# Performance work log

Measured on AMD Instinct MI355X. Metric: run time of the kernel, lower is better.

The kernel has to match this reference:

```python
import jax, jax.numpy as jnp
import numpy as np

B, S, D, H = 4, 2048, 1024, 16
HD = D // H  # 64


def setup_inputs() -> dict:
    key = jax.random.key(0)
    ks = jax.random.split(key, 8)
    s = 0.02
    return {
        "inp_values": jax.random.normal(ks[0], (B, S, D), jnp.float32),
        "inp_keys": jax.random.normal(ks[1], (B, S, D), jnp.float32),
        "inp_queries": jax.random.normal(ks[2], (B, S, D), jnp.float32),
        # per-head projection weights, torch nn.Linear(head_dims, head_dims, bias=False): y = x @ W.T
        "Wv": jax.random.normal(ks[3], (HD, HD), jnp.float32) * s,
        "Wk": jax.random.normal(ks[4], (HD, HD), jnp.float32) * s,
        "Wq": jax.random.normal(ks[5], (HD, HD), jnp.float32) * s,
        # output projection nn.Linear(D, D) with bias
        "Wo": jax.random.normal(ks[6], (D, D), jnp.float32) * s,
        "bo": jax.random.normal(ks[7], (D,), jnp.float32) * s,
    }


def reference(inp_values, inp_keys, inp_queries, Wv, Wk, Wq, Wo, bo):
    b, sq, _ = inp_queries.shape
    sk = inp_values.shape[1]
    v = inp_values.reshape(b, sk, H, HD)
    k = inp_keys.reshape(b, sk, H, HD)
    q = inp_queries.reshape(b, sq, H, HD)
    # per-head linear: x @ W.T
    v = jnp.einsum('bshd,ed->bshe', v, Wv)
    k = jnp.einsum('bshd,ed->bshe', k, Wk)
    q = jnp.einsum('bshd,ed->bshe', q, Wq)
    # scores scaled by 1/sqrt(input_dims) as in the original (not head_dims)
    scores = jnp.einsum('bqhd,bkhd->bhqk', q, k) / jnp.sqrt(jnp.float32(D))
    attn = jax.nn.softmax(scores, axis=-1)  # [B,H,Q,K]
    out = jnp.einsum('bhqk,bkhd->bqhd', attn, v).reshape(b, sq, D)
    return out @ Wo.T + bo
```

## Files before the change

### kernel.cpp

```cpp
#include <hip/hip_runtime.h>
#include <hip/hip_bf16.h>

#define B_ 4
#define S_ 2048
#define D_ 1024
#define H_ 16
#define HD_ 64

typedef __attribute__((ext_vector_type(8))) short bf16x8;
typedef __attribute__((ext_vector_type(4))) float f32x4;

#define MFMA32(a, b, c) __builtin_amdgcn_mfma_f32_16x16x32_bf16(a, b, c, 0, 0, 0)

#define KSWZ(r) ((((r) & 3)) ^ ((((r) >> 3) & 1) << 2))

__device__ __forceinline__ float fast_exp2(float x) {
#if __has_builtin(__builtin_amdgcn_exp2f)
  return __builtin_amdgcn_exp2f(x);
#else
  return exp2f(x);
#endif
}

__device__ __forceinline__ float fast_rcp(float x) {
#if __has_builtin(__builtin_amdgcn_rcpf)
  return __builtin_amdgcn_rcpf(x);
#else
  return 1.0f / x;
#endif
}

__device__ __forceinline__ short f2bf(float x) {
  union { float f; unsigned u; } v; v.f = x;
  unsigned r = (v.u + 0x7fffu + ((v.u >> 16) & 1u)) >> 16;
  return (short)(r & 0xffffu);
}

__device__ __forceinline__ unsigned pack_hi16(float a, float b) {
  union { float f; unsigned u; } ua, ub; ua.f = a; ub.f = b;
  return __builtin_amdgcn_perm(ub.u, ua.u, 0x07060302u);
}

__device__ __forceinline__ void gl_lds16(const short* g, void* l) {
  __builtin_amdgcn_global_load_lds(
      (const __attribute__((address_space(1))) unsigned*)(const void*)g,
      (__attribute__((address_space(3))) unsigned*)l, 16, 0, 0);
}

__global__ __launch_bounds__(256) void qkv_proj2(
    const float* __restrict__ inpV, const float* __restrict__ inpK,
    const float* __restrict__ inpQ, const float* __restrict__ Wv,
    const float* __restrict__ Wk, const float* __restrict__ Wq,
    const float* __restrict__ Wo, short* __restrict__ wob,
    short* __restrict__ vt, short* __restrict__ kp, short* __restrict__ qp) {
  __shared__ bf16x8 xbuf[1024];
  __shared__ bf16x8 wbuf[512];
  int bid = blockIdx.x;
  int t = bid >> 10;
  int tid = threadIdx.x, wave = tid >> 6, lane = tid & 63;
  int quad = lane >> 4, l15 = lane & 15;

  if (t == 3) {
    int i = (bid & 511) * 256 + tid;
    const float4* src = (const float4*)Wo + i * 2;
    float4 a = src[0], b = src[1];
    bf16x8 o;
    o[0] = f2bf(a.x); o[1] = f2bf(a.y); o[2] = f2bf(a.z); o[3] = f2bf(a.w);
    o[4] = f2bf(b.x); o[5] = f2bf(b.y); o[6] = f2bf(b.z); o[7] = f2bf(b.w);
    ((bf16x8*)wob)[i] = o;
    return;
  }

  int bh = (bid >> 4) & 63;
  int st = bid & 15;
  int b = bh >> 4, h = bh & 15;
  int s0 = st * 128;
  const float* inp = (t == 0) ? inpV : (t == 1) ? inpK : inpQ;
  const float* W = (t == 0) ? Wv : (t == 1) ? Wk : Wq;
  float wscale = (t == 2) ? (0.03125f * 1.4426950408889634f) : 1.0f;

#pragma unroll
  for (int u = 0; u < 2; ++u) {
    int slot = tid + u * 256;
    int row = slot >> 3, g = slot & 7;
    const float4* wp = (const float4*)(W + row * 64 + g * 8);
    float4 w0 = wp[0], w1 = wp[1];
    bf16x8 o;
    o[0] = f2bf(w0.x * wscale); o[1] = f2bf(w0.y * wscale);
    o[2] = f2bf(w0.z * wscale); o[3] = f2bf(w0.w * wscale);
    o[4] = f2bf(w1.x * wscale); o[5] = f2bf(w1.y * wscale);
    o[6] = f2bf(w1.z * wscale); o[7] = f2bf(w1.w * wscale);
    wbuf[row * 8 + (g ^ (row & 7))] = o;
  }
  const float* xg = inp + (b * S_ + s0) * D_ + h * HD_;
#pragma unroll
  for (int u = 0; u < 4; ++u) {
    int slot = tid + u * 256;
    int row = slot >> 3, g = slot & 7;
    const float4* xp = (const float4*)(xg + row * D_ + g * 8);
    float4 x0 = xp[0], x1 = xp[1];
    bf16x8 o;
    o[0] = f2bf(x0.x); o[1] = f2bf(x0.y); o[2] = f2bf(x0.z); o[3] = f2bf(x0.w);
    o[4] = f2bf(x1.x); o[5] = f2bf(x1.y); o[6] = f2bf(x1.z); o[7] = f2bf(x1.w);
    xbuf[row * 8 + (g ^ (row & 7))] = o;
  }
  __syncthreads();

  if (t == 0) {
    f32x4 acc[4][2];
#pragma unroll
    for (int mt = 0; mt < 4; mt++)
#pragma unroll
      for (int nt = 0; nt < 2; nt++) { acc[mt][nt][0]=0.f; acc[mt][nt][1]=0.f; acc[mt][nt][2]=0.f; acc[mt][nt][3]=0.f; }
#pragma unroll
    for (int ks = 0; ks < 2; ++ks) {
      bf16x8 af[4], bfr[2];
#pragma unroll
      for (int mt = 0; mt < 4; ++mt) {
        int row = mt * 16 + l15;
        af[mt] = wbuf[row * 8 + ((ks * 4 + quad) ^ (row & 7))];
      }
#pragma unroll
      for (int nt = 0; nt < 2; ++nt) {
        int row = wave * 32 + nt * 16 + l15;
        bfr[nt] = xbuf[row * 8 + ((ks * 4 + quad) ^ (row & 7))];
      }
#pragma unroll
      for (int mt = 0; mt < 4; ++mt)
#pragma unroll
        for (int nt = 0; nt < 2; ++nt)
          acc[mt][nt] = MFMA32(af[mt], bfr[nt], acc[mt][nt]);
    }
    short* vb = vt + (bh * 64) * S_ + s0 + wave * 32;
#pragma unroll
    for (int mt = 0; mt < 4; ++mt)
#pragma unroll
      for (int nt = 0; nt < 2; ++nt)
#pragma unroll
        for (int r = 0; r < 4; ++r) {
          int e = mt * 16 + quad * 4 + r;
          int s = nt * 16 + l15;
          vb[e * S_ + s] = f2bf(acc[mt][nt][r]);
        }
  } else {
    f32x4 acc[2][4];
#pragma unroll
    for (int mt = 0; mt < 2; mt++)
#pragma unroll
      for (int nt = 0; nt < 4; nt++) { acc[mt][nt][0]=0.f; acc[mt][nt][1]=0.f; acc[mt][nt][2]=0.f; acc[mt][nt][3]=0.f; }
#pragma unroll
    for (int ks = 0; ks < 2; ++ks) {
      bf16x8 af[2], bfr[4];
#pragma unroll
      for (int mt = 0; mt < 2; ++mt) {
        int row = wave * 32 + mt * 16 + l15;
        af[mt] = xbuf[row * 8 + ((ks * 4 + quad) ^ (row & 7))];
      }
#pragma unroll
      for (int nt = 0; nt < 4; ++nt) {
        int row = nt * 16 + l15;
        bfr[nt] = wbuf[row * 8 + ((ks * 4 + quad) ^ (row & 7))];
      }
#pragma unroll
      for (int mt = 0; mt < 2; ++mt)
#pragma unroll
        for (int nt = 0; nt < 4; ++nt)
          acc[mt][nt] = MFMA32(af[mt], bfr[nt], acc[mt][nt]);
    }
    short* ob = ((t == 1) ? kp : qp) + (bh * S_ + s0 + wave * 32) * 64;
#pragma unroll
    for (int mt = 0; mt < 2; ++mt)
#pragma unroll
      for (int nt = 0; nt < 4; ++nt)
#pragma unroll
        for (int r = 0; r < 4; ++r) {
          int s = mt * 16 + quad * 4 + r;
          int e = nt * 16 + l15;
          ob[s * 64 + e] = f2bf(acc[mt][nt][r]);
        }
  }
}

__global__ __launch_bounds__(128, 4) void attention(
    const short* __restrict__ qp, const short* __restrict__ kp,
    const short* __restrict__ vt, short* __restrict__ ao) {
  __shared__ bf16x8 kbuf[2][256];
  __shared__ bf16x8 vbuf[2][256];
  int bid = blockIdx.x;
  int qt = bid >> 6;
  int bh = bid & 63;
  int tid = threadIdx.x, wave = tid >> 6, lane = tid & 63;
  int quad = lane >> 4, l15 = lane & 15;

  const short* qb = qp + (bh * S_ + qt * 64 + wave * 32 + l15) * 64;
  bf16x8 bq[2][2];
  bq[0][0] = *(const bf16x8*)(qb + quad * 8);
  bq[0][1] = *(const bf16x8*)(qb + 32 + quad * 8);
  bq[1][0] = *(const bf16x8*)(qb + 1024 + quad * 8);
  bq[1][1] = *(const bf16x8*)(qb + 1024 + 32 + quad * 8);

  const f32x4 fzero = {0.f, 0.f, 0.f, 0.f};
  f32x4 o[2][4];
#pragma unroll
  for (int g = 0; g < 2; g++)
#pragma unroll
    for (int dt = 0; dt < 4; dt++) o[g][dt] = fzero;
  f32x4 lacc[2];
  lacc[0] = fzero; lacc[1] = fzero;

  short one_bf = (short)0x3F80;
  bf16x8 ones8;
#pragma unroll
  for (int j = 0; j < 8; ++j) ones8[j] = (l15 == 0) ? one_bf : (short)0;

  const short* kg = kp + bh * S_ * 64;
  const short* vg = vt + bh * 64 * S_;

  int krow0 = tid >> 3, kg0 = (tid & 7) ^ KSWZ(krow0);
  int krow1 = (tid + 128) >> 3, kg1 = (tid & 7) ^ KSWZ(krow1);
  const short* kA = kg + krow0 * 64 + kg0 * 8;
  const short* kB = kg + krow1 * 64 + kg1 * 8;
  int vrow0 = tid >> 2, vg0 = (tid & 3) ^ (vrow0 & 3);
  int vrow1 = (tid + 128) >> 2, vg1 = (tid & 3) ^ (vrow1 & 3);
  const short* vA = vg + vrow0 * S_ + vg0 * 8;
  const short* vB = vg + vrow1 * S_ + vg1 * 8;

  gl_lds16(kA, &kbuf[0][tid]);
  gl_lds16(kB, &kbuf[0][tid + 128]);
  gl_lds16(vA, &vbuf[0][tid]);
  gl_lds16(vB, &vbuf[0][tid + 128]);

  int krp0 = ((l15 >> 2) << 3) + (l15 & 3);

  int aslot0[2], aslot1[2], vslot[4];
#pragma unroll
  for (int nt = 0; nt < 2; ++nt) {
    int krow = krp0 + nt * 4;
    aslot0[nt] = krow * 8 + ((0 + quad) ^ KSWZ(krow));
    aslot1[nt] = krow * 8 + ((4 + quad) ^ KSWZ(krow));
  }
#pragma unroll
  for (int dt = 0; dt < 4; ++dt) {
    int d = dt * 16 + l15;
    vslot[dt] = d * 4 + (quad ^ (d & 3));
  }

#define ATTN_BODY(P, T)                                                     \
  do {                                                                      \
    __syncthreads();                                                        \
    int ktn = ((T) + 1) & 63;                                               \
    gl_lds16(kA + ktn * 2048, &kbuf[(P) ^ 1][tid]);                         \
    gl_lds16(kB + ktn * 2048, &kbuf[(P) ^ 1][tid + 128]);                   \
    gl_lds16(vA + ktn * 32, &vbuf[(P) ^ 1][tid]);                           \
    gl_lds16(vB + ktn * 32, &vbuf[(P) ^ 1][tid + 128]);                     \
    union Frag { unsigned u[4]; bf16x8 v; } pa0, pa1;                       \
    _Pragma("unroll")                                                       \
    for (int nt = 0; nt < 2; ++nt) {                                        \
      bf16x8 ak0 = kbuf[(P)][aslot0[nt]];                                   \
      bf16x8 ak1 = kbuf[(P)][aslot1[nt]];                                   \
      f32x4 c0 = MFMA32(ak0, bq[0][0], fzero);                              \
      f32x4 c1 = MFMA32(ak0, bq[1][0], fzero);                              \
      c0 = MFMA32(ak1, bq[0][1], c0);                                       \
      c1 = MFMA32(ak1, bq[1][1], c1);                                       \
      float e00 = fast_exp2(c0[0]), e01 = fast_exp2(c0[1]);                 \
      float e02 = fast_exp2(c0[2]), e03 = fast_exp2(c0[3]);                 \
      float e10 = fast_exp2(c1[0]), e11 = fast_exp2(c1[1]);                 \
      float e12 = fast_exp2(c1[2]), e13 = fast_exp2(c1[3]);                 \
      pa0.u[nt * 2 + 0] = pack_hi16(e00, e01);                              \
      pa0.u[nt * 2 + 1] = pack_hi16(e02, e03);                              \
      pa1.u[nt * 2 + 0] = pack_hi16(e10, e11);                              \
      pa1.u[nt * 2 + 1] = pack_hi16(e12, e13);                              \
    }                                                                       \
    __builtin_amdgcn_s_setprio(1);                                          \
    lacc[0] = MFMA32(pa0.v, ones8, lacc[0]);                                \
    lacc[1] = MFMA32(pa1.v, ones8, lacc[1]);                                \
    _Pragma("unroll")                                                       \
    for (int dt = 0; dt < 4; ++dt) {                                        \
      bf16x8 bv = vbuf[(P)][vslot[dt]];                                     \
      o[0][dt] = MFMA32(pa0.v, bv, o[0][dt]);                               \
      o[1][dt] = MFMA32(pa1.v, bv, o[1][dt]);                               \
    }                                                                       \
    __builtin_amdgcn_s_setprio(0);                                          \
  } while (0)

  for (int kt = 0; kt < 64; kt += 2) {
    ATTN_BODY(0, kt);
    ATTN_BODY(1, kt + 1);
  }
#undef ATTN_BODY

  int b = bh >> 4, h = bh & 15;
#pragma unroll
  for (int g = 0; g < 2; ++g) {
    float inv[4];
#pragma unroll
    for (int r = 0; r < 4; ++r) {
      float ls = __shfl(lacc[g][r], lane & 48, 64);
      inv[r] = fast_rcp(ls);
    }
#pragma unroll
    for (int dt = 0; dt < 4; ++dt)
#pragma unroll
      for (int r = 0; r < 4; ++r) {
        int srow = qt * 64 + wave * 32 + g * 16 + quad * 4 + r;
        ao[(b * S_ + srow) * D_ + h * 64 + dt * 16 + l15] =
            f2bf(o[g][dt][r] * inv[r]);
      }
  }
}

__global__ __launch_bounds__(256) void outproj(const short* __restrict__ A,
                                               const short* __restrict__ Bw,
                                               const float* __restrict__ bo,
                                               float* __restrict__ out) {
  __shared__ bf16x8 sa[2][1024];
  __shared__ bf16x8 sb[2][1024];
  int bid = blockIdx.x;
  int m0 = (bid >> 3) * 128, n0 = (bid & 7) * 128;
  int tid = threadIdx.x, wave = tid >> 6, lane = tid & 63;
  int quad = lane >> 4, l15 = lane & 15;
  int wm = (wave >> 1) * 64, wn = (wave & 1) * 64;
  f32x4 acc[4][4];
#pragma unroll
  for (int mt = 0; mt < 4; mt++)
#pragma unroll
    for (int nt = 0; nt < 4; nt++) { acc[mt][nt][0]=0.f; acc[mt][nt][1]=0.f; acc[mt][nt][2]=0.f; acc[mt][nt][3]=0.f; }

  const short* asrc[4];
  const short* bsrc[4];
#pragma unroll
  for (int u = 0; u < 4; ++u) {
    int slot = tid + u * 256;
    int row = slot >> 3, g = (slot & 7) ^ (row & 7);
    asrc[u] = A + (m0 + row) * 1024 + g * 8;
    bsrc[u] = Bw + (n0 + row) * 1024 + g * 8;
  }
#pragma unroll
  for (int u = 0; u < 4; ++u) {
    gl_lds16(asrc[u], &sa[0][tid + u * 256]);
    gl_lds16(bsrc[u], &sb[0][tid + u * 256]);
  }

  int p = 0;
  for (int k0 = 0; k0 < 1024; k0 += 64) {
    __syncthreads();
    int kn = (k0 + 64) & 1023;
#pragma unroll
    for (int u = 0; u < 4; ++u) {
      gl_lds16(asrc[u] + kn, &sa[p ^ 1][tid + u * 256]);
      gl_lds16(bsrc[u] + kn, &sb[p ^ 1][tid + u * 256]);
    }
#pragma unroll
    for (int ks = 0; ks < 2; ++ks) {
      bf16x8 af[4], bf[4];
#pragma unroll
      for (int mt = 0; mt < 4; ++mt) {
        int row = wm + mt * 16 + l15;
        af[mt] = sa[p][row * 8 + ((ks * 4 + quad) ^ (row & 7))];
      }
#pragma unroll
      for (int nt = 0; nt < 4; ++nt) {
        int row = wn + nt * 16 + l15;
        bf[nt] = sb[p][row * 8 + ((ks * 4 + quad) ^ (row & 7))];
      }
#pragma unroll
      for (int mt = 0; mt < 4; ++mt)
#pragma unroll
        for (int nt = 0; nt < 4; ++nt)
          acc[mt][nt] = MFMA32(af[mt], bf[nt], acc[mt][nt]);
    }
    p ^= 1;
  }
#pragma unroll
  for (int nt = 0; nt < 4; ++nt) {
    int n = n0 + wn + nt * 16 + l15;
    float bov = bo[n];
#pragma unroll
    for (int mt = 0; mt < 4; ++mt)
#pragma unroll
      for (int r = 0; r < 4; r++) {
        int m = m0 + wm + mt * 16 + quad * 4 + r;
        out[m * 1024 + n] = acc[mt][nt][r] + bov;
      }
  }
}

extern "C" void kernel_launch(void* const* d_in, const int* in_sizes, int n_in,
                              void* d_out, int out_size, void* d_ws,
                              size_t ws_size, hipStream_t stream) {
  const float* inpV = (const float*)d_in[0];
  const float* inpK = (const float*)d_in[1];
  const float* inpQ = (const float*)d_in[2];
  const float* Wv = (const float*)d_in[3];
  const float* Wk = (const float*)d_in[4];
  const float* Wq = (const float*)d_in[5];
  const float* Wo = (const float*)d_in[6];
  const float* bo = (const float*)d_in[7];
  float* out = (float*)d_out;

  char* ws = (char*)d_ws;
  short* vt = (short*)(ws);
  short* kp = (short*)(ws + (16u << 20));
  short* qp = (short*)(ws + (32u << 20));
  short* ao = (short*)(ws + (48u << 20));
  short* wob = (short*)(ws + (64u << 20));

  qkv_proj2<<<dim3(3584), dim3(256), 0, stream>>>(inpV, inpK, inpQ, Wv, Wk, Wq,
                                                  Wo, wob, vt, kp, qp);
  attention<<<dim3(2048), dim3(128), 0, stream>>>(qp, kp, vt, ao);
  outproj<<<dim3(512), dim3(256), 0, stream>>>(ao, wob, bo, out);
}
```

Baseline: 265.0 us.

## Use single-wave attention blocks handling 64 queries with vmcnt-based sync

The attention kernel now runs one wave per block, and that wave processes all 64 query rows as four 16-row groups. Previously two waves split 32 rows each. Each K/V fragment read from LDS is therefore reused across four query groups. Because the block has a single wave, the __syncthreads barrier is replaced with an explicit s_waitcnt vmcnt on the async global-to-LDS copies. The cost is more accumulator and Q registers per thread and half the waves per block, which may lower latency hiding. The waitcnt(8) logic also depends on how the compiler counts issued loads.

```diff
diff --git a/kernel.cpp b/kernel.cpp
--- a/kernel.cpp
+++ b/kernel.cpp
@@ -181,7 +181,7 @@
   }
 }
 
-__global__ __launch_bounds__(128, 4) void attention(
+__global__ __launch_bounds__(64, 2) void attention(
     const short* __restrict__ qp, const short* __restrict__ kp,
     const short* __restrict__ vt, short* __restrict__ ao) {
   __shared__ bf16x8 kbuf[2][256];
@@ -189,24 +189,26 @@
   int bid = blockIdx.x;
   int qt = bid >> 6;
   int bh = bid & 63;
-  int tid = threadIdx.x, wave = tid >> 6, lane = tid & 63;
+  int lane = threadIdx.x & 63;
   int quad = lane >> 4, l15 = lane & 15;
 
-  const short* qb = qp + (bh * S_ + qt * 64 + wave * 32 + l15) * 64;
-  bf16x8 bq[2][2];
-  bq[0][0] = *(const bf16x8*)(qb + quad * 8);
-  bq[0][1] = *(const bf16x8*)(qb + 32 + quad * 8);
-  bq[1][0] = *(const bf16x8*)(qb + 1024 + quad * 8);
-  bq[1][1] = *(const bf16x8*)(qb + 1024 + 32 + quad * 8);
+  const short* qb = qp + (bh * S_ + qt * 64 + l15) * 64;
+  bf16x8 bq[4][2];
+#pragma unroll
+  for (int qg = 0; qg < 4; ++qg) {
+    bq[qg][0] = *(const bf16x8*)(qb + qg * 1024 + quad * 8);
+    bq[qg][1] = *(const bf16x8*)(qb + qg * 1024 + 32 + quad * 8);
+  }
 
   const f32x4 fzero = {0.f, 0.f, 0.f, 0.f};
-  f32x4 o[2][4];
-#pragma unroll
-  for (int g = 0; g < 2; g++)
-#pragma unroll
-    for (int dt = 0; dt < 4; dt++) o[g][dt] = fzero;
-  f32x4 lacc[2];
-  lacc[0] = fzero; lacc[1] = fzero;
+  f32x4 o[4][4];
+#pragma unroll
+  for (int qg = 0; qg < 4; qg++)
+#pragma unroll
+    for (int dt = 0; dt < 4; dt++) o[qg][dt] = fzero;
+  f32x4 lacc[4];
+#pragma unroll
+  for (int qg = 0; qg < 4; qg++) lacc[qg] = fzero;
 
   short one_bf = (short)0x3F80;
   bf16x8 ones8;
@@ -216,19 +218,21 @@
   const short* kg = kp + bh * S_ * 64;
   const short* vg = vt + bh * 64 * S_;
 
-  int krow0 = tid >> 3, kg0 = (tid & 7) ^ KSWZ(krow0);
-  int krow1 = (tid + 128) >> 3, kg1 = (tid & 7) ^ KSWZ(krow1);
-  const short* kA = kg + krow0 * 64 + kg0 * 8;
-  const short* kB = kg + krow1 * 64 + kg1 * 8;
-  int vrow0 = tid >> 2, vg0 = (tid & 3) ^ (vrow0 & 3);
-  int vrow1 = (tid + 128) >> 2, vg1 = (tid & 3) ^ (vrow1 & 3);
-  const short* vA = vg + vrow0 * S_ + vg0 * 8;
-  const short* vB = vg + vrow1 * S_ + vg1 * 8;
-
-  gl_lds16(kA, &kbuf[0][tid]);
-  gl_lds16(kB, &kbuf[0][tid + 128]);
-  gl_lds16(vA, &vbuf[0][tid]);
-  gl_lds16(vB, &vbuf[0][tid + 128]);
+  const short* ksrc[4];
+  const short* vsrc[4];
+#pragma unroll
+  for (int u = 0; u < 4; ++u) {
+    int slot = lane + u * 64;
+    int kr = slot >> 3, kgg = (slot & 7) ^ KSWZ(kr);
+    ksrc[u] = kg + kr * 64 + kgg * 8;
+    int vr = slot >> 2, vgg = (slot & 3) ^ (vr & 3);
+    vsrc[u] = vg + vr * S_ + vgg * 8;
+  }
+
+#pragma unroll
+  for (int u = 0; u < 4; ++u) gl_lds16(ksrc[u], &kbuf[0][u * 64]);
+#pragma unroll
+  for (int u = 0; u < 4; ++u) gl_lds16(vsrc[u], &vbuf[0][u * 64]);
 
   int krp0 = ((l15 >> 2) << 3) + (l15 & 3);
 
@@ -247,38 +251,40 @@
 
 #define ATTN_BODY(P, T)                                                     \
   do {                                                                      \
-    __syncthreads();                                                        \
-    int ktn = ((T) + 1) & 63;                                               \
-    gl_lds16(kA + ktn * 2048, &kbuf[(P) ^ 1][tid]);                         \
-    gl_lds16(kB + ktn * 2048, &kbuf[(P) ^ 1][tid + 128]);                   \
-    gl_lds16(vA + ktn * 32, &vbuf[(P) ^ 1][tid]);                           \
-    gl_lds16(vB + ktn * 32, &vbuf[(P) ^ 1][tid + 128]);                     \
-    union Frag { unsigned u[4]; bf16x8 v; } pa0, pa1;                       \
+    int ktn = ((T) + 1) & 63; \
+    _Pragma("unroll")                                                       \
+    for (int u = 0; u < 4; ++u)                                             \
+      gl_lds16(ksrc[u] + ktn * 2048, &kbuf[(P) ^ 1][u * 64]);               \
+    _Pragma("unroll")                                                       \
+    for (int u = 0; u < 4; ++u)                                             \
+      gl_lds16(vsrc[u] + ktn * 32, &vbuf[(P) ^ 1][u * 64]);                 \
+    asm volatile("s_waitcnt vmcnt(8)" ::: "memory");     \
+    __builtin_amdgcn_sched_barrier(0);                                      \
+    union Frag { unsigned u[4]; bf16x8 v; } pa[4];                          \
     _Pragma("unroll")                                                       \
     for (int nt = 0; nt < 2; ++nt) {                                        \
       bf16x8 ak0 = kbuf[(P)][aslot0[nt]];                                   \
       bf16x8 ak1 = kbuf[(P)][aslot1[nt]];                                   \
-      f32x4 c0 = MFMA32(ak0, bq[0][0], fzero);                              \
-      f32x4 c1 = MFMA32(ak0, bq[1][0], fzero);                              \
-      c0 = MFMA32(ak1, bq[0][1], c0);                                       \
-      c1 = MFMA32(ak1, bq[1][1], c1);                                       \
-      float e00 = fast_exp2(c0[0]), e01 = fast_exp2(c0[1]);                 \
-      float e02 = fast_exp2(c0[2]), e03 = fast_exp2(c0[3]);                 \
-      float e10 = fast_exp2(c1[0]), e11 = fast_exp2(c1[1]);                 \
-      float e12 = fast_exp2(c1[2]), e13 = fast_exp2(c1[3]);                 \
-      pa0.u[nt * 2 + 0] = pack_hi16(e00, e01);                              \
-      pa0.u[nt * 2 + 1] = pack_hi16(e02, e03);                              \
-      pa1.u[nt * 2 + 0] = pack_hi16(e10, e11);                              \
-      pa1.u[nt * 2 + 1] = pack_hi16(e12, e13);                              \
+      _Pragma("unroll")                                                     \
+      for (int qg = 0; qg < 4; ++qg) {                                      \
+        f32x4 c = MFMA32(ak0, bq[qg][0], fzero);                            \
+        c = MFMA32(ak1, bq[qg][1], c);                                      \
+        float e0 = fast_exp2(c[0]), e1 = fast_exp2(c[1]);                   \
+        float e2 = fast_exp2(c[2]), e3 = fast_exp2(c[3]);                   \
+        pa[qg].u[nt * 2 + 0] = pack_hi16(e0, e1);                           \
+        pa[qg].u[nt * 2 + 1] = pack_hi16(e2, e3);                           \
+      }                                                                     \
     }                                                                       \
     __builtin_amdgcn_s_setprio(1);                                          \
-    lacc[0] = MFMA32(pa0.v, ones8, lacc[0]);                                \
-    lacc[1] = MFMA32(pa1.v, ones8, lacc[1]);                                \
+    _Pragma("unroll")                                                       \
+    for (int qg = 0; qg < 4; ++qg)                                          \
+      lacc[qg] = MFMA32(pa[qg].v, ones8, lacc[qg]);                         \
     _Pragma("unroll")                                                       \
     for (int dt = 0; dt < 4; ++dt) {                                        \
       bf16x8 bv = vbuf[(P)][vslot[dt]];                                     \
-      o[0][dt] = MFMA32(pa0.v, bv, o[0][dt]);                               \
-      o[1][dt] = MFMA32(pa1.v, bv, o[1][dt]);                               \
+      _Pragma("unroll")                                                     \
+      for (int qg = 0; qg < 4; ++qg)                                        \
+        o[qg][dt] = MFMA32(pa[qg].v, bv, o[qg][dt]);                        \
     }                                                                       \
     __builtin_amdgcn_s_setprio(0);                                          \
   } while (0)
@@ -289,22 +295,24 @@
   }
 #undef ATTN_BODY
 
+  asm volatile("s_waitcnt vmcnt(0)" ::: "memory");
+
   int b = bh >> 4, h = bh & 15;
 #pragma unroll
-  for (int g = 0; g < 2; ++g) {
+  for (int qg = 0; qg < 4; ++qg) {
     float inv[4];
 #pragma unroll
     for (int r = 0; r < 4; ++r) {
-      float ls = __shfl(lacc[g][r], lane & 48, 64);
+      float ls = __shfl(lacc[qg][r], lane & 48, 64);
       inv[r] = fast_rcp(ls);
     }
 #pragma unroll
     for (int dt = 0; dt < 4; ++dt)
 #pragma unroll
       for (int r = 0; r < 4; ++r) {
-        int srow = qt * 64 + wave * 32 + g * 16 + quad * 4 + r;
+        int srow = qt * 64 + qg * 16 + quad * 4 + r;
         ao[(b * S_ + srow) * D_ + h * 64 + dt * 16 + l15] =
-            f2bf(o[g][dt][r] * inv[r]);
+            f2bf(o[qg][dt][r] * inv[r]);
       }
   }
 }
@@ -407,6 +415,6 @@
 
   qkv_proj2<<<dim3(3584), dim3(256), 0, stream>>>(inpV, inpK, inpQ, Wv, Wk, Wq,
                                                   Wo, wob, vt, kp, qp);
-  attention<<<dim3(2048), dim3(128), 0, stream>>>(qp, kp, vt, ao);
+  attention<<<dim3(2048), dim3(64), 0, stream>>>(qp, kp, vt, ao);
   outproj<<<dim3(512), dim3(256), 0, stream>>>(ao, wob, bo, out);
 }
```

After: 261.8 us. Within noise of the previous version (-1.2%).

## Load K/V fragments directly from global into registers, drop LDS staging

Applied to the files above, without the earlier changes.

The attention kernel no longer stages K and V tiles in shared memory with barriers. Each single-wave block now loads its MFMA operand fragments straight from global memory into registers, double-buffering K across iterations, and the grid becomes 4096 blocks of 64 threads. This removes the __syncthreads and LDS traffic, but K/V reuse across waves now relies on the L2/L1 caches. Global loads use strided 16-byte accesses that may coalesce less well, and extra register buffers may reduce occupancy.

```diff
diff --git a/kernel.cpp b/kernel.cpp
--- a/kernel.cpp
+++ b/kernel.cpp
@@ -11,8 +11,6 @@
 typedef __attribute__((ext_vector_type(4))) float f32x4;
 
 #define MFMA32(a, b, c) __builtin_amdgcn_mfma_f32_16x16x32_bf16(a, b, c, 0, 0, 0)
-
-#define KSWZ(r) ((((r) & 3)) ^ ((((r) >> 3) & 1) << 2))
 
 __device__ __forceinline__ float fast_exp2(float x) {
 #if __has_builtin(__builtin_amdgcn_exp2f)
@@ -181,30 +179,29 @@
   }
 }
 
-__global__ __launch_bounds__(128, 4) void attention(
+__global__ __launch_bounds__(64, 3) void attention(
     const short* __restrict__ qp, const short* __restrict__ kp,
     const short* __restrict__ vt, short* __restrict__ ao) {
-  __shared__ bf16x8 kbuf[2][256];
-  __shared__ bf16x8 vbuf[2][256];
   int bid = blockIdx.x;
   int qt = bid >> 6;
   int bh = bid & 63;
-  int tid = threadIdx.x, wave = tid >> 6, lane = tid & 63;
+  int lane = threadIdx.x & 63;
   int quad = lane >> 4, l15 = lane & 15;
 
-  const short* qb = qp + (bh * S_ + qt * 64 + wave * 32 + l15) * 64;
+  const short* qb = qp + (bh * S_ + qt * 32 + l15) * 64;
   bf16x8 bq[2][2];
-  bq[0][0] = *(const bf16x8*)(qb + quad * 8);
-  bq[0][1] = *(const bf16x8*)(qb + 32 + quad * 8);
-  bq[1][0] = *(const bf16x8*)(qb + 1024 + quad * 8);
-  bq[1][1] = *(const bf16x8*)(qb + 1024 + 32 + quad * 8);
+#pragma unroll
+  for (int qg = 0; qg < 2; ++qg) {
+    bq[qg][0] = *(const bf16x8*)(qb + qg * 1024 + quad * 8);
+    bq[qg][1] = *(const bf16x8*)(qb + qg * 1024 + 32 + quad * 8);
+  }
 
   const f32x4 fzero = {0.f, 0.f, 0.f, 0.f};
   f32x4 o[2][4];
 #pragma unroll
-  for (int g = 0; g < 2; g++)
-#pragma unroll
-    for (int dt = 0; dt < 4; dt++) o[g][dt] = fzero;
+  for (int qg = 0; qg < 2; qg++)
+#pragma unroll
+    for (int dt = 0; dt < 4; dt++) o[qg][dt] = fzero;
   f32x4 lacc[2];
   lacc[0] = fzero; lacc[1] = fzero;
 
@@ -213,55 +210,40 @@
 #pragma unroll
   for (int j = 0; j < 8; ++j) ones8[j] = (l15 == 0) ? one_bf : (short)0;
 
-  const short* kg = kp + bh * S_ * 64;
-  const short* vg = vt + bh * 64 * S_;
-
-  int krow0 = tid >> 3, kg0 = (tid & 7) ^ KSWZ(krow0);
-  int krow1 = (tid + 128) >> 3, kg1 = (tid & 7) ^ KSWZ(krow1);
-  const short* kA = kg + krow0 * 64 + kg0 * 8;
-  const short* kB = kg + krow1 * 64 + kg1 * 8;
-  int vrow0 = tid >> 2, vg0 = (tid & 3) ^ (vrow0 & 3);
-  int vrow1 = (tid + 128) >> 2, vg1 = (tid & 3) ^ (vrow1 & 3);
-  const short* vA = vg + vrow0 * S_ + vg0 * 8;
-  const short* vB = vg + vrow1 * S_ + vg1 * 8;
-
-  gl_lds16(kA, &kbuf[0][tid]);
-  gl_lds16(kB, &kbuf[0][tid + 128]);
-  gl_lds16(vA, &vbuf[0][tid]);
-  gl_lds16(vB, &vbuf[0][tid + 128]);
-
   int krp0 = ((l15 >> 2) << 3) + (l15 & 3);
 
-  int aslot0[2], aslot1[2], vslot[4];
-#pragma unroll
-  for (int nt = 0; nt < 2; ++nt) {
-    int krow = krp0 + nt * 4;
-    aslot0[nt] = krow * 8 + ((0 + quad) ^ KSWZ(krow));
-    aslot1[nt] = krow * 8 + ((4 + quad) ^ KSWZ(krow));
-  }
-#pragma unroll
-  for (int dt = 0; dt < 4; ++dt) {
-    int d = dt * 16 + l15;
-    vslot[dt] = d * 4 + (quad ^ (d & 3));
-  }
-
-#define ATTN_BODY(P, T)                                                     \
-  do {                                                                      \
-    __syncthreads();                                                        \
-    int ktn = ((T) + 1) & 63;                                               \
-    gl_lds16(kA + ktn * 2048, &kbuf[(P) ^ 1][tid]);                         \
-    gl_lds16(kB + ktn * 2048, &kbuf[(P) ^ 1][tid + 128]);                   \
-    gl_lds16(vA + ktn * 32, &vbuf[(P) ^ 1][tid]);                           \
-    gl_lds16(vB + ktn * 32, &vbuf[(P) ^ 1][tid + 128]);                     \
+  const short* kptr = kp + bh * (S_ * 64) + krp0 * 64 + quad * 8;
+  const short* vp0 = vt + bh * (64 * S_) + l15 * S_ + quad * 8;
+  const short* vp1 = vp0 + 16 * S_;
+  const short* vp2 = vp0 + 32 * S_;
+  const short* vp3 = vp0 + 48 * S_;
+
+  bf16x8 akA[2][2], akB[2][2], bv[4];
+
+#define ISSUE_K(SET) do {                                                   \
+    ak##SET[0][0] = *(const bf16x8*)(kptr);                                 \
+    ak##SET[0][1] = *(const bf16x8*)(kptr + 32);                            \
+    ak##SET[1][0] = *(const bf16x8*)(kptr + 256);                           \
+    ak##SET[1][1] = *(const bf16x8*)(kptr + 288);                           \
+    kptr += 2048;                                                           \
+  } while (0)
+
+#define ISSUE_V() do {                                                      \
+    bv[0] = *(const bf16x8*)(vp0);                                          \
+    bv[1] = *(const bf16x8*)(vp1);                                          \
+    bv[2] = *(const bf16x8*)(vp2);                                          \
+    bv[3] = *(const bf16x8*)(vp3);                                          \
+    vp0 += 32; vp1 += 32; vp2 += 32; vp3 += 32;                             \
+  } while (0)
+
+#define COMPUTE(SET) do {                                                   \
     union Frag { unsigned u[4]; bf16x8 v; } pa0, pa1;                       \
     _Pragma("unroll")                                                       \
     for (int nt = 0; nt < 2; ++nt) {                                        \
-      bf16x8 ak0 = kbuf[(P)][aslot0[nt]];                                   \
-      bf16x8 ak1 = kbuf[(P)][aslot1[nt]];                                   \
-      f32x4 c0 = MFMA32(ak0, bq[0][0], fzero);                              \
-      f32x4 c1 = MFMA32(ak0, bq[1][0], fzero);                              \
-      c0 = MFMA32(ak1, bq[0][1], c0);                                       \
-      c1 = MFMA32(ak1, bq[1][1], c1);                                       \
+      f32x4 c0 = MFMA32(ak##SET[nt][0], bq[0][0], fzero);                   \
+      f32x4 c1 = MFMA32(ak##SET[nt][0], bq[1][0], fzero);                   \
+      c0 = MFMA32(ak##SET[nt][1], bq[0][1], c0);                            \
+      c1 = MFMA32(ak##SET[nt][1], bq[1][1], c1);                            \
       float e00 = fast_exp2(c0[0]), e01 = fast_exp2(c0[1]);                 \
       float e02 = fast_exp2(c0[2]), e03 = fast_exp2(c0[3]);                 \
       float e10 = fast_exp2(c1[0]), e11 = fast_exp2(c1[1]);                 \
@@ -276,35 +258,43 @@
     lacc[1] = MFMA32(pa1.v, ones8, lacc[1]);                                \
     _Pragma("unroll")                                                       \
     for (int dt = 0; dt < 4; ++dt) {                                        \
-      bf16x8 bv = vbuf[(P)][vslot[dt]];                                     \
-      o[0][dt] = MFMA32(pa0.v, bv, o[0][dt]);                               \
-      o[1][dt] = MFMA32(pa1.v, bv, o[1][dt]);                               \
+      o[0][dt] = MFMA32(pa0.v, bv[dt], o[0][dt]);                           \
+      o[1][dt] = MFMA32(pa1.v, bv[dt], o[1][dt]);                           \
     }                                                                       \
     __builtin_amdgcn_s_setprio(0);                                          \
   } while (0)
 
+  ISSUE_K(A);
   for (int kt = 0; kt < 64; kt += 2) {
-    ATTN_BODY(0, kt);
-    ATTN_BODY(1, kt + 1);
-  }
-#undef ATTN_BODY
+    ISSUE_V();
+    ISSUE_K(B);
+    __builtin_amdgcn_sched_barrier(0);
+    COMPUTE(A);
+    ISSUE_V();
+    ISSUE_K(A);
+    __builtin_amdgcn_sched_barrier(0);
+    COMPUTE(B);
+  }
+#undef ISSUE_K
+#undef ISSUE_V
+#undef COMPUTE
 
   int b = bh >> 4, h = bh & 15;
 #pragma unroll
-  for (int g = 0; g < 2; ++g) {
+  for (int qg = 0; qg < 2; ++qg) {
     float inv[4];
 #pragma unroll
     for (int r = 0; r < 4; ++r) {
-      float ls = __shfl(lacc[g][r], lane & 48, 64);
+      float ls = __shfl(lacc[qg][r], lane & 48, 64);
       inv[r] = fast_rcp(ls);
     }
 #pragma unroll
     for (int dt = 0; dt < 4; ++dt)
 #pragma unroll
       for (int r = 0; r < 4; ++r) {
-        int srow = qt * 64 + wave * 32 + g * 16 + quad * 4 + r;
+        int srow = qt * 32 + qg * 16 + quad * 4 + r;
         ao[(b * S_ + srow) * D_ + h * 64 + dt * 16 + l15] =
-            f2bf(o[g][dt][r] * inv[r]);
+            f2bf(o[qg][dt][r] * inv[r]);
       }
   }
 }
@@ -407,6 +397,6 @@
 
   qkv_proj2<<<dim3(3584), dim3(256), 0, stream>>>(inpV, inpK, inpQ, Wv, Wk, Wq,
                                                   Wo, wob, vt, kp, qp);
-  attention<<<dim3(2048), dim3(128), 0, stream>>>(qp, kp, vt, ao);
+  attention<<<dim3(4096), dim3(64), 0, stream>>>(qp, kp, vt, ao);
   outproj<<<dim3(512), dim3(256), 0, stream>>>(ao, wob, bo, out);
 }
```

New measurement: 422.7 us. 1.59x slower.
